# Kernel tuning notes

Measured on AMD Instinct MI355X. Metric: run time of the kernel, lower is better.

## Reference

```python
import jax, jax.numpy as jnp
import numpy as np

N_NODES = 100000
SELF_LOOP_W = 2.0  # improved=True in GCNConv -> A + 2I


def gcn_conv(x, src, dst, ew, W, b):
    """PyG GCNConv(improved=True): D^-1/2 (A + 2I) D^-1/2 X W + b.

    src/dst: edge endpoints, messages flow src -> dst (source_to_target).
    """
    n = x.shape[0]
    # degree after adding self loops with weight 2.0
    deg = jnp.zeros((n,), dtype=x.dtype).at[dst].add(ew) + SELF_LOOP_W
    dinv = jax.lax.rsqrt(deg)
    norm = dinv[src] * ew * dinv[dst]                      # [E]
    h = x @ W                                              # [N, out]
    agg = jax.ops.segment_sum(norm[:, None] * h[src], dst, num_segments=n)
    self_term = (SELF_LOOP_W * dinv * dinv)[:, None] * h   # self-loop edges
    return agg + self_term + b


def setup_inputs() -> dict:
    key = jax.random.key(0)
    ks = jax.random.split(key, 10)
    F_IN, H1, H2, C = 128, 128, 64, 5
    E = 1600000
    x = jax.random.normal(ks[0], (N_NODES, F_IN), dtype=jnp.float32)
    edge_index = jax.random.randint(ks[1], (2, E), 0, N_NODES, dtype=jnp.int64)
    edge_weight = jax.random.uniform(ks[2], (E,), dtype=jnp.float32)

    def glorot(k, shape):
        lim = float(np.sqrt(6.0 / (shape[0] + shape[1])))
        return jax.random.uniform(k, shape, jnp.float32, -lim, lim)

    return {
        "x": x,
        "edge_index": edge_index,
        "edge_weight": edge_weight,
        "W1": glorot(ks[3], (F_IN, H1)), "b1": jnp.zeros((H1,), jnp.float32),
        "W2": glorot(ks[4], (H1, H2)),  "b2": jnp.zeros((H2,), jnp.float32),
        "Wc": glorot(ks[5], (H2, C)),   "bc": jnp.zeros((C,), jnp.float32),
    }


def reference(x, edge_index, edge_weight, W1, b1, W2, b2, Wc, bc):
    src, dst = edge_index[0], edge_index[1]
    # conv1 + relu (dropout is identity in eval mode)
    h = jax.nn.relu(gcn_conv(x, src, dst, edge_weight, W1, b1))
    # conv2 + relu
    h = jax.nn.relu(gcn_conv(h, src, dst, edge_weight, W2, b2))
    # classifier head + log_softmax over classes
    logits = gcn_conv(h, src, dst, edge_weight, Wc, bc)
    return jax.nn.log_softmax(logits, axis=1)
```

## Files before the change

kernel.cpp:

```cpp
#include <hip/hip_runtime.h>
#include <hip/hip_bf16.h>

constexpr int TPB = 256;

static inline int cdiv(long long a, long long b) { return (int)((a + b - 1) / b); }

typedef __attribute__((ext_vector_type(8))) short bf16x8;
typedef __attribute__((ext_vector_type(4))) float f32x4;

__device__ inline unsigned short f2bf(float f) {
    __hip_bfloat16 h = __float2bfloat16(f);
    unsigned short u;
    __builtin_memcpy(&u, &h, 2);
    return u;
}

__device__ inline float bflo(unsigned u) { return __uint_as_float(u << 16); }
__device__ inline float bfhi(unsigned u) { return __uint_as_float(u & 0xffff0000u); }

__device__ inline unsigned relu_pk(unsigned w) {
    unsigned lo = (w & 0x8000u) ? 0u : (w & 0xFFFFu);
    unsigned hi = (w & 0x80000000u) ? 0u : (w & 0xFFFF0000u);
    return lo | hi;
}

constexpr int P1_CH   = 4096;
constexpr int MAXBINS = 512;
constexpr int BINCAP  = 4608;

__device__ __forceinline__ void part_body(const int* __restrict__ src,
                                          const int* __restrict__ dst,
                                          const float* __restrict__ ew,
                                          int* __restrict__ bincnt,
                                          int2* __restrict__ pbuf, int E, int nbins, int bid) {
    __shared__ int h[MAXBINS];
    for (int t = threadIdx.x; t < nbins; t += TPB) h[t] = 0;
    __syncthreads();
    const int lo = bid * P1_CH;
    const int hi = min(lo + P1_CH, E);
    for (int e = lo + threadIdx.x; e < hi; e += TPB)
        atomicAdd(&h[dst[e] >> 8], 1);
    __syncthreads();
    for (int t = threadIdx.x; t < nbins; t += TPB) {
        int c = h[t];
        h[t] = (c > 0) ? atomicAdd(&bincnt[t], c) : 0;
    }
    __syncthreads();
    for (int e = lo + threadIdx.x; e < hi; e += TPB) {
        int d = dst[e];
        int bin = d >> 8;
        int idx = atomicAdd(&h[bin], 1);
        if (idx < BINCAP)
            pbuf[(size_t)bin * BINCAP + idx] =
                make_int2((src[e] & 0x1FFFF) | ((d & 255) << 24), __float_as_int(ew[e]));
    }
}

template<int CAP>
__global__ __launch_bounds__(TPB) void k_bucket(const int2* __restrict__ pbuf,
                                                const int* __restrict__ bincnt,
                                                int2* __restrict__ pairs,
                                                int* __restrict__ cnt,
                                                float* __restrict__ dinv, int n) {
    __shared__ int   lcnt[TPB];
    __shared__ float ldeg[TPB];
    const int tid = threadIdx.x;
    lcnt[tid] = 0; ldeg[tid] = 0.f;
    __syncthreads();
    const int bin = blockIdx.x;
    const int m = min(bincnt[bin], BINCAP);
    const int2* pb = pbuf + (size_t)bin * BINCAP;
    for (int i = tid; i < m; i += TPB) {
        int2 pe = pb[i];
        int dlo = (pe.x >> 24) & 255;
        int s   = pe.x & 0x1FFFF;
        int pos = atomicAdd(&lcnt[dlo], 1);
        if (pos < CAP)
            pairs[(size_t)(bin * 256 + dlo) * CAP + pos] = make_int2(s, pe.y);
        atomicAdd(&ldeg[dlo], __int_as_float(pe.y));
    }
    __syncthreads();
    int node = bin * 256 + tid;
    if (node < n) {
        cnt[node]  = min(lcnt[tid], CAP);
        dinv[node] = rsqrtf(ldeg[tid] + 2.0f);
    }
}

template<int CAP>
__global__ void k_bucket_scatter(const int* __restrict__ src, const int* __restrict__ dst,
                                 const float* __restrict__ ew, int* __restrict__ cnt,
                                 int2* __restrict__ pairs, int E) {
    int e = blockIdx.x * TPB + threadIdx.x;
    if (e >= E) return;
    int d = dst[e];
    int pos = atomicAdd(&cnt[d], 1);
    if (pos < CAP)
        pairs[(size_t)d * CAP + pos] = make_int2(src[e], __float_as_int(ew[e]));
}

template<int CAP>
__global__ void k_deg(const int2* __restrict__ pairs, const int* __restrict__ cnt,
                      float* __restrict__ dinv, int n) {
    int node = blockIdx.x * (TPB / 64) + (threadIdx.x >> 6);
    if (node >= n) return;
    int lane = threadIdx.x & 63;
    int m = min(cnt[node], CAP);
    float v = 0.f;
    if (lane < m) v = __int_as_float(pairs[(size_t)node * CAP + lane].y);
#pragma unroll
    for (int d = 1; d < 64; d <<= 1) v += __shfl_xor(v, d);
    if (lane == 0) dinv[node] = rsqrtf(v + 2.0f);
}

template<int CAP>
__global__ void k_normw(int2* __restrict__ pairs, const int* __restrict__ cnt,
                        const float* __restrict__ dinv, int n) {
    int lane = threadIdx.x & 63;
    int g = lane >> 4, o = lane & 15;
    int wid = blockIdx.x * (TPB / 64) + (threadIdx.x >> 6);
    int node = wid * 4 + g;
    if (node >= n) return;
    int m = min(cnt[node], CAP);
    float dd = dinv[node];
    int2* pr = pairs + (size_t)node * CAP;
    for (int j = o; j < m; j += 16) {
        int2 p = pr[j];
        pr[j].y = __float_as_int(dinv[p.x] * __int_as_float(p.y) * dd);
    }
}

__global__ void k_prepw(const float* __restrict__ W1, const float* __restrict__ W2,
                        __hip_bfloat16* __restrict__ Wt1, __hip_bfloat16* __restrict__ Wt2) {
    int i = blockIdx.x * TPB + threadIdx.x;
    if (i < 128 * 128) {
        int k = i >> 7, c = i & 127;
        Wt1[c * 128 + k] = __float2bfloat16(W1[i]);
    }
    if (i < 128 * 64) {
        int k = i >> 6, c = i & 63;
        Wt2[c * 128 + k] = __float2bfloat16(W2[i]);
    }
}


template<int KIN, int NCOL, bool RELU_IN, bool BF_IN>
__device__ __forceinline__ void gemm_mfma_body(const void* __restrict__ Xv,
                                               const __hip_bfloat16* __restrict__ Wt,
                                               __hip_bfloat16* __restrict__ H, int n, int bid) {
    constexpr int BM  = 128;
    constexpr int SX  = KIN + 8;
    constexpr int KCH = KIN / 32;
    constexpr int MT  = 4;
    constexpr int NT  = NCOL / 32;
    __shared__ short Xs[BM * SX];
    __shared__ short Ws[NCOL * SX];

    const int row0 = bid * BM;
    const int nrow = min(BM, n - row0);

    if constexpr (BF_IN) {
        const uint4* xg = (const uint4*)((const __hip_bfloat16*)Xv + (size_t)row0 * KIN);
        for (int i = threadIdx.x; i < BM * KIN / 8; i += TPB) {
            int r = i / (KIN / 8), c8 = i % (KIN / 8);
            uint4 v = make_uint4(0u, 0u, 0u, 0u);
            if (r < nrow) v = xg[i];
            if (RELU_IN) {
                v.x = relu_pk(v.x); v.y = relu_pk(v.y);
                v.z = relu_pk(v.z); v.w = relu_pk(v.w);
            }
            *(uint4*)&Xs[r * SX + c8 * 8] = v;
        }
    } else {
        const float4* xg = (const float4*)((const float*)Xv + (size_t)row0 * KIN);
        for (int i = threadIdx.x; i < BM * KIN / 4; i += TPB) {
            int r = i / (KIN / 4), c4 = i % (KIN / 4);
            float4 v = make_float4(0.f, 0.f, 0.f, 0.f);
            if (r < nrow) v = xg[i];
            if (RELU_IN) {
                v.x = fmaxf(v.x, 0.f); v.y = fmaxf(v.y, 0.f);
                v.z = fmaxf(v.z, 0.f); v.w = fmaxf(v.w, 0.f);
            }
            ushort4 b;
            b.x = f2bf(v.x); b.y = f2bf(v.y);
            b.z = f2bf(v.z); b.w = f2bf(v.w);
            *(ushort4*)&Xs[r * SX + c4 * 4] = b;
        }
    }
    {
        const uint4* wg = (const uint4*)Wt;
        for (int i = threadIdx.x; i < NCOL * KIN / 8; i += TPB) {
            int c = i / (KIN / 8), k8 = i % (KIN / 8);
            *(uint4*)&Ws[c * SX + k8 * 8] = wg[i];
        }
    }
    __syncthreads();

    const int wave = threadIdx.x >> 6;
    const int lane = threadIdx.x & 63;
    const int wr = wave >> 1;
    const int wc = wave & 1;
    const int fr = lane & 15;
    const int fg = lane >> 4;

    f32x4 acc[MT][NT];
#pragma unroll
    for (int i = 0; i < MT; ++i)
#pragma unroll
        for (int j = 0; j < NT; ++j) acc[i][j] = (f32x4){0.f, 0.f, 0.f, 0.f};

    const short* xa = Xs + (wr * 64 + fr) * SX + fg * 8;
    const short* wb = Ws + (wc * NT * 16 + fr) * SX + fg * 8;

#pragma unroll
    for (int kc = 0; kc < KCH; ++kc) {
        bf16x8 a[MT], b[NT];
#pragma unroll
        for (int i = 0; i < MT; ++i)
            a[i] = *(const bf16x8*)(xa + i * 16 * SX + kc * 32);
#pragma unroll
        for (int j = 0; j < NT; ++j)
            b[j] = *(const bf16x8*)(wb + j * 16 * SX + kc * 32);
#pragma unroll
        for (int i = 0; i < MT; ++i)
#pragma unroll
            for (int j = 0; j < NT; ++j)
                acc[i][j] = __builtin_amdgcn_mfma_f32_16x16x32_bf16(a[i], b[j], acc[i][j], 0, 0, 0);
    }

#pragma unroll
    for (int i = 0; i < MT; ++i) {
#pragma unroll
        for (int j = 0; j < NT; ++j) {
            int col = wc * NT * 16 + j * 16 + fr;
            int rb  = wr * 64 + i * 16 + fg * 4;
#pragma unroll
            for (int q = 0; q < 4; ++q) {
                int r = rb + q;
                if (r < nrow)
                    H[(size_t)(row0 + r) * NCOL + col] = __float2bfloat16(acc[i][j][q]);
            }
        }
    }
}

template<int KIN, int NCOL, bool RELU_IN, bool BF_IN>
__global__ __launch_bounds__(TPB, 2) void k_gemm_mfma(const void* __restrict__ Xv,
                                                      const __hip_bfloat16* __restrict__ Wt,
                                                      __hip_bfloat16* __restrict__ H, int n) {
    gemm_mfma_body<KIN, NCOL, RELU_IN, BF_IN>(Xv, Wt, H, n, blockIdx.x);
}

__global__ __launch_bounds__(TPB, 2) void k_gemm1_part(
        const float* __restrict__ X, const __hip_bfloat16* __restrict__ Wt1,
        __hip_bfloat16* __restrict__ H, int n,
        const int* __restrict__ src, const int* __restrict__ dst,
        const float* __restrict__ ew, int* __restrict__ bincnt,
        int2* __restrict__ pbuf, int E, int nbins, int Gg, int Gp) {
    int b = blockIdx.x;
    int r3 = b % 3;
    if (r3 == 2) {
        int pid = b / 3;
        if (pid < Gp) part_body(src, dst, ew, bincnt, pbuf, E, nbins, pid);
    } else {
        int gid = (b / 3) * 2 + r3;
        if (gid < Gg) gemm_mfma_body<128, 128, false, false>(X, Wt1, H, n, gid);
    }
}

template<int KIN, int KOUT, int OSTR, bool RELU_IN>
__global__ void k_gemv(const float* __restrict__ X, const float* __restrict__ W,
                       float* __restrict__ H, int n) {
    __shared__ float ws_[KIN * KOUT];
    for (int i = threadIdx.x; i < KIN * KOUT; i += TPB) ws_[i] = W[i];
    __syncthreads();
    int r = blockIdx.x * TPB + threadIdx.x;
    if (r >= n) return;
    float acc[KOUT];
#pragma unroll
    for (int c = 0; c < KOUT; ++c) acc[c] = 0.f;
    const float4* xr = (const float4*)(X + (size_t)r * KIN);
#pragma unroll
    for (int k4 = 0; k4 < KIN / 4; ++k4) {
        float4 xv = xr[k4];
        if (RELU_IN) {
            xv.x = fmaxf(xv.x, 0.f); xv.y = fmaxf(xv.y, 0.f);
            xv.z = fmaxf(xv.z, 0.f); xv.w = fmaxf(xv.w, 0.f);
        }
        float xs[4] = {xv.x, xv.y, xv.z, xv.w};
#pragma unroll
        for (int j = 0; j < 4; ++j)
#pragma unroll
            for (int c = 0; c < KOUT; ++c)
                acc[c] = fmaf(xs[j], ws_[(k4 * 4 + j) * KOUT + c], acc[c]);
    }
#pragma unroll
    for (int c = 0; c < KOUT; ++c) H[(size_t)r * OSTR + c] = acc[c];
#pragma unroll
    for (int c = KOUT; c < OSTR; ++c) H[(size_t)r * OSTR + c] = 0.f;
}


template<int K, int CAP, bool OUT_BF16>
__global__ __launch_bounds__(TPB) void k_agg_bf(const __hip_bfloat16* __restrict__ H,
                                                const int2* __restrict__ pairs,
                                                const int* __restrict__ cnt,
                                                const float* __restrict__ dinv,
                                                const float* __restrict__ b,
                                                void* __restrict__ out, int n) {
    constexpr int LPN = K / 8;
    constexpr int GPN = 64 / LPN;
    constexpr int RQ  = K / 8;
    constexpr int NCH = CAP / 8;
    const int lane = threadIdx.x & 63;
    const int g    = lane / LPN;
    const int o    = lane % LPN;
    const int wid  = blockIdx.x * (TPB / 64) + (threadIdx.x >> 6);
    const int node = wid * GPN + g;
    const bool alive = node < n;
    const int nc = alive ? node : 0;

    const uint4* __restrict__ Hq = (const uint4*)H;

    float di   = dinv[nc];
    float coef = 2.f * di * di;
    uint4 hv = Hq[(size_t)nc * RQ + o];
    const float4* bq = (const float4*)b + o * 2;
    float4 bA = bq[0], bB = bq[1];
    float acc[8];
    acc[0] = fmaf(coef, bflo(hv.x), bA.x);
    acc[1] = fmaf(coef, bfhi(hv.x), bA.y);
    acc[2] = fmaf(coef, bflo(hv.y), bA.z);
    acc[3] = fmaf(coef, bfhi(hv.y), bA.w);
    acc[4] = fmaf(coef, bflo(hv.z), bB.x);
    acc[5] = fmaf(coef, bfhi(hv.z), bB.y);
    acc[6] = fmaf(coef, bflo(hv.w), bB.z);
    acc[7] = fmaf(coef, bfhi(hv.w), bB.w);

    const int m = alive ? min(cnt[nc], CAP) : 0;
    const int2* pp = pairs + (size_t)nc * CAP;

    uint4 Ma[4], Mb[4];
#pragma unroll
    for (int q = 0; q < 4; ++q) Ma[q] = *(const uint4*)(pp + q * 2);

    auto chunk = [&](const uint4 (&Mc)[4], uint4 (&Mn)[4], int c) {
        const int base = c * 8;
        int s[8]; float w[8];
#pragma unroll
        for (int q = 0; q < 4; ++q) {
            s[2 * q]     = (int)Mc[q].x;  w[2 * q]     = __uint_as_float(Mc[q].y);
            s[2 * q + 1] = (int)Mc[q].z;  w[2 * q + 1] = __uint_as_float(Mc[q].w);
        }
        uint4 r[8];
#pragma unroll
        for (int u = 0; u < 8; ++u) {
            bool ok = (base + u) < m;
            int ss = ok ? s[u] : 0;
            if (!ok) w[u] = 0.f;
            r[u] = Hq[(size_t)ss * RQ + o];
        }
        if (base + 8 < m) {
#pragma unroll
            for (int q = 0; q < 4; ++q) Mn[q] = *(const uint4*)(pp + base + 8 + q * 2);
        }
#pragma unroll
        for (int u = 0; u < 8; ++u) {
            acc[0] = fmaf(w[u], bflo(r[u].x), acc[0]);
            acc[1] = fmaf(w[u], bfhi(r[u].x), acc[1]);
            acc[2] = fmaf(w[u], bflo(r[u].y), acc[2]);
            acc[3] = fmaf(w[u], bfhi(r[u].y), acc[3]);
            acc[4] = fmaf(w[u], bflo(r[u].z), acc[4]);
            acc[5] = fmaf(w[u], bfhi(r[u].z), acc[5]);
            acc[6] = fmaf(w[u], bflo(r[u].w), acc[6]);
            acc[7] = fmaf(w[u], bfhi(r[u].w), acc[7]);
        }
    };

#pragma unroll
    for (int c = 0; c < NCH; c += 2) {
        if (c * 8 >= m) break;
        chunk(Ma, Mb, c);
        if ((c + 1) * 8 >= m) break;
        chunk(Mb, Ma, c + 1);
    }

    if (alive) {
        if constexpr (OUT_BF16) {
            unsigned p0 = (unsigned)f2bf(acc[0]) | ((unsigned)f2bf(acc[1]) << 16);
            unsigned p1 = (unsigned)f2bf(acc[2]) | ((unsigned)f2bf(acc[3]) << 16);
            unsigned p2 = (unsigned)f2bf(acc[4]) | ((unsigned)f2bf(acc[5]) << 16);
            unsigned p3 = (unsigned)f2bf(acc[6]) | ((unsigned)f2bf(acc[7]) << 16);
            ((uint4*)out)[(size_t)node * RQ + o] = make_uint4(p0, p1, p2, p3);
        } else {
            float4* ap = (float4*)out + (size_t)node * (K / 4) + o * 2;
            ap[0] = make_float4(acc[0], acc[1], acc[2], acc[3]);
            ap[1] = make_float4(acc[4], acc[5], acc[6], acc[7]);
        }
    }
}

template<int CAP>
__global__ void k_agg5_lsm(const float* __restrict__ H, const int2* __restrict__ pairs,
                           const int* __restrict__ cnt, const float* __restrict__ dinv,
                           const float* __restrict__ b, float* __restrict__ out, int n) {
    constexpr int NCH = CAP / 8;
    int i = blockIdx.x * TPB + threadIdx.x;
    const bool alive = i < n;
    const int nc = alive ? i : 0;
    float di = dinv[nc];
    float coef = 2.f * di * di;
    float acc[5];
    {
        const float4 h0 = *(const float4*)(H + (size_t)nc * 8);
        const float  h4 = H[(size_t)nc * 8 + 4];
        acc[0] = fmaf(coef, h0.x, b[0]);
        acc[1] = fmaf(coef, h0.y, b[1]);
        acc[2] = fmaf(coef, h0.z, b[2]);
        acc[3] = fmaf(coef, h0.w, b[3]);
        acc[4] = fmaf(coef, h4,   b[4]);
    }
    const int m = alive ? min(cnt[nc], CAP) : 0;
    const int2* pp = pairs + (size_t)nc * CAP;

    uint4 Ma[4], Mb[4];
#pragma unroll
    for (int q = 0; q < 4; ++q) Ma[q] = *(const uint4*)(pp + q * 2);

    auto chunk = [&](const uint4 (&Mc)[4], uint4 (&Mn)[4], int c) {
        const int base = c * 8;
        int s[8]; float w[8];
#pragma unroll
        for (int q = 0; q < 4; ++q) {
            s[2 * q]     = (int)Mc[q].x;  w[2 * q]     = __uint_as_float(Mc[q].y);
            s[2 * q + 1] = (int)Mc[q].z;  w[2 * q + 1] = __uint_as_float(Mc[q].w);
        }
        float4 q0[8]; float q4[8];
#pragma unroll
        for (int u = 0; u < 8; ++u) {
            bool ok = (base + u) < m;
            int ss = ok ? s[u] : 0;
            if (!ok) w[u] = 0.f;
            const float* h = H + (size_t)ss * 8;
            q0[u] = *(const float4*)h;
            q4[u] = h[4];
        }
        if (base + 8 < m) {
#pragma unroll
            for (int q = 0; q < 4; ++q) Mn[q] = *(const uint4*)(pp + base + 8 + q * 2);
        }
#pragma unroll
        for (int u = 0; u < 8; ++u) {
            acc[0] = fmaf(w[u], q0[u].x, acc[0]);
            acc[1] = fmaf(w[u], q0[u].y, acc[1]);
            acc[2] = fmaf(w[u], q0[u].z, acc[2]);
            acc[3] = fmaf(w[u], q0[u].w, acc[3]);
            acc[4] = fmaf(w[u], q4[u],   acc[4]);
        }
    };

#pragma unroll
    for (int c = 0; c < NCH; c += 2) {
        if (c * 8 >= m) break;
        chunk(Ma, Mb, c);
        if ((c + 1) * 8 >= m) break;
        chunk(Mb, Ma, c + 1);
    }

    if (alive) {
        float mx = acc[0];
#pragma unroll
        for (int c = 1; c < 5; ++c) mx = fmaxf(mx, acc[c]);
        float ssum = 0.f;
#pragma unroll
        for (int c = 0; c < 5; ++c) ssum += expf(acc[c] - mx);
        float lg = mx + logf(ssum);
#pragma unroll
        for (int c = 0; c < 5; ++c) out[(size_t)i * 5 + c] = acc[c] - lg;
    }
}


template<int CAP>
static void run_all(const float* x, const int* srcv, const int* dstv, const float* ew,
                    const float* W1, const float* b1, const float* W2, const float* b2,
                    const float* Wc, const float* bc, float* out,
                    int n, int E, char* p, hipStream_t stream) {
    auto alloc = [&](size_t bytes) {
        char* r = p;
        p += (bytes + 255) & ~(size_t)255;
        return r;
    };
    float*          dinv   = (float*)alloc((size_t)n * 4);
    int*            cnt    = (int*)alloc((size_t)n * 4);
    int2*           pairs  = (int2*)alloc((size_t)n * CAP * 8);
    __hip_bfloat16* Hbf    = (__hip_bfloat16*)alloc((size_t)n * 128 * 2);
    __hip_bfloat16* A1bf   = (__hip_bfloat16*)alloc((size_t)n * 128 * 2);
    float*          bufB   = (float*)alloc((size_t)n * 64 * 4);
    float*          H3     = (float*)alloc((size_t)n * 8 * 4);
    int*            bincnt = (int*)alloc((size_t)MAXBINS * 4);
    int2*           pbuf   = (int2*)alloc((size_t)MAXBINS * BINCAP * 8);
    __hip_bfloat16* Wt1    = (__hip_bfloat16*)alloc(128 * 128 * 2);
    __hip_bfloat16* Wt2    = (__hip_bfloat16*)alloc(128 * 64 * 2);

    const int WPB = TPB / 64;
    const int nbins = cdiv(n, 256);

    k_prepw<<<cdiv(128 * 128, TPB), TPB, 0, stream>>>(W1, W2, Wt1, Wt2);

    if (nbins <= MAXBINS) {
        (void)hipMemsetAsync(bincnt, 0, (size_t)nbins * 4, stream);
        int Gg = cdiv(n, 128);
        int Gp = cdiv(E, P1_CH);
        int Gh = cdiv(Gg, 2);
        int G  = 3 * (Gp > Gh ? Gp : Gh);
        k_gemm1_part<<<G, TPB, 0, stream>>>(x, Wt1, Hbf, n, srcv, dstv, ew,
                                            bincnt, pbuf, E, nbins, Gg, Gp);
        k_bucket<CAP><<<nbins, TPB, 0, stream>>>(pbuf, bincnt, pairs, cnt, dinv, n);
    } else {
        (void)hipMemsetAsync(cnt, 0, (size_t)n * 4, stream);
        k_bucket_scatter<CAP><<<cdiv(E, TPB), TPB, 0, stream>>>(srcv, dstv, ew, cnt, pairs, E);
        k_deg<CAP><<<cdiv(n, WPB), TPB, 0, stream>>>(pairs, cnt, dinv, n);
        k_gemm_mfma<128, 128, false, false><<<cdiv(n, 128), TPB, 0, stream>>>(x, Wt1, Hbf, n);
    }
    k_normw<CAP><<<cdiv(n, WPB * 4), TPB, 0, stream>>>(pairs, cnt, dinv, n);

    k_agg_bf<128, CAP, true><<<cdiv(n, WPB * 4), TPB, 0, stream>>>(Hbf, pairs, cnt, dinv, b1, A1bf, n);

    k_gemm_mfma<128, 64, true, true><<<cdiv(n, 128), TPB, 0, stream>>>(A1bf, Wt2, Hbf, n);
    k_agg_bf<64, CAP, false><<<cdiv(n, WPB * 8), TPB, 0, stream>>>(Hbf, pairs, cnt, dinv, b2, bufB, n);

    k_gemv<64, 5, 8, true><<<cdiv(n, TPB), TPB, 0, stream>>>(bufB, Wc, H3, n);
    k_agg5_lsm<CAP><<<cdiv(n, TPB), TPB, 0, stream>>>(H3, pairs, cnt, dinv, bc, out, n);
}

extern "C" void kernel_launch(void* const* d_in, const int* in_sizes, int n_in,
                              void* d_out, int out_size, void* d_ws, size_t ws_size,
                              hipStream_t stream) {
    const float* x  = (const float*)d_in[0];
    const int*   ei = (const int*)d_in[1];
    const float* ew = (const float*)d_in[2];
    const float* W1 = (const float*)d_in[3];
    const float* b1 = (const float*)d_in[4];
    const float* W2 = (const float*)d_in[5];
    const float* b2 = (const float*)d_in[6];
    const float* Wc = (const float*)d_in[7];
    const float* bc = (const float*)d_in[8];

    const int E   = in_sizes[2];
    const int H1  = in_sizes[4];
    const int FIN = in_sizes[3] / H1;
    const int n   = in_sizes[0] / FIN;

    const int* srcv = ei;
    const int* dstv = ei + E;

    size_t fixed = ((size_t)n * 4 + 256) * 2 + ((size_t)n * 128 * 2 + 256) * 2 +
                   (size_t)n * 64 * 4 + 256 + (size_t)n * 8 * 4 + 256 +
                   (size_t)MAXBINS * 4 + 256 + (size_t)MAXBINS * BINCAP * 8 + 256 +
                   128 * 128 * 2 + 256 + 128 * 64 * 2 + 256 + 1024;
    if (ws_size == 0 || ws_size >= fixed + (size_t)n * 64 * 8)
        run_all<64>(x, srcv, dstv, ew, W1, b1, W2, b2, Wc, bc, (float*)d_out, n, E,
                    (char*)d_ws, stream);
    else
        run_all<48>(x, srcv, dstv, ew, W1, b1, W2, b2, Wc, bc, (float*)d_out, n, E,
                    (char*)d_ws, stream);
}
```

Before: 216.7 us.

## Load GEMM weights directly from global with register prefetch, cut LDS, raise occupancy

Drops the shared-memory staging of the weight matrix in the MFMA GEMM. B fragments are now read directly from global (L2-cached) memory, with a one-step register double buffer. The fused gemm+partition kernel shares a single LDS buffer between its two roles, and launch bounds go from 2 to 4 blocks per SM to raise occupancy. The trade-off is more global and L2 traffic per wave and more register pressure under the tighter launch bound.

```diff
diff --git a/kernel.cpp b/kernel.cpp
--- a/kernel.cpp
+++ b/kernel.cpp
@@ -32,8 +32,8 @@
                                           const int* __restrict__ dst,
                                           const float* __restrict__ ew,
                                           int* __restrict__ bincnt,
-                                          int2* __restrict__ pbuf, int E, int nbins, int bid) {
-    __shared__ int h[MAXBINS];
+                                          int2* __restrict__ pbuf, int E, int nbins,
+                                          int* h, int bid) {
     for (int t = threadIdx.x; t < nbins; t += TPB) h[t] = 0;
     __syncthreads();
     const int lo = bid * P1_CH;
@@ -147,14 +147,13 @@
 template<int KIN, int NCOL, bool RELU_IN, bool BF_IN>
 __device__ __forceinline__ void gemm_mfma_body(const void* __restrict__ Xv,
                                                const __hip_bfloat16* __restrict__ Wt,
-                                               __hip_bfloat16* __restrict__ H, int n, int bid) {
+                                               __hip_bfloat16* __restrict__ H, int n,
+                                               int bid, short* Xs) {
     constexpr int BM  = 128;
     constexpr int SX  = KIN + 8;
     constexpr int KCH = KIN / 32;
     constexpr int MT  = 4;
     constexpr int NT  = NCOL / 32;
-    __shared__ short Xs[BM * SX];
-    __shared__ short Ws[NCOL * SX];
 
     const int row0 = bid * BM;
     const int nrow = min(BM, n - row0);
@@ -187,13 +186,6 @@
             *(ushort4*)&Xs[r * SX + c4 * 4] = b;
         }
     }
-    {
-        const uint4* wg = (const uint4*)Wt;
-        for (int i = threadIdx.x; i < NCOL * KIN / 8; i += TPB) {
-            int c = i / (KIN / 8), k8 = i % (KIN / 8);
-            *(uint4*)&Ws[c * SX + k8 * 8] = wg[i];
-        }
-    }
     __syncthreads();
 
     const int wave = threadIdx.x >> 6;
@@ -210,22 +202,33 @@
         for (int j = 0; j < NT; ++j) acc[i][j] = (f32x4){0.f, 0.f, 0.f, 0.f};
 
     const short* xa = Xs + (wr * 64 + fr) * SX + fg * 8;
-    const short* wb = Ws + (wc * NT * 16 + fr) * SX + fg * 8;
+    const __hip_bfloat16* wg = Wt + (size_t)(wc * NT * 16 + fr) * KIN + fg * 8;
+
+    bf16x8 bcur[NT], bnxt[NT];
+#pragma unroll
+    for (int j = 0; j < NT; ++j)
+        bcur[j] = *(const bf16x8*)(wg + (size_t)j * 16 * KIN);
 
 #pragma unroll
     for (int kc = 0; kc < KCH; ++kc) {
-        bf16x8 a[MT], b[NT];
+        bf16x8 a[MT];
 #pragma unroll
         for (int i = 0; i < MT; ++i)
             a[i] = *(const bf16x8*)(xa + i * 16 * SX + kc * 32);
-#pragma unroll
-        for (int j = 0; j < NT; ++j)
-            b[j] = *(const bf16x8*)(wb + j * 16 * SX + kc * 32);
+        if (kc + 1 < KCH) {
+#pragma unroll
+            for (int j = 0; j < NT; ++j)
+                bnxt[j] = *(const bf16x8*)(wg + (size_t)j * 16 * KIN + (kc + 1) * 32);
+        }
 #pragma unroll
         for (int i = 0; i < MT; ++i)
 #pragma unroll
             for (int j = 0; j < NT; ++j)
-                acc[i][j] = __builtin_amdgcn_mfma_f32_16x16x32_bf16(a[i], b[j], acc[i][j], 0, 0, 0);
+                acc[i][j] = __builtin_amdgcn_mfma_f32_16x16x32_bf16(a[i], bcur[j], acc[i][j], 0, 0, 0);
+        if (kc + 1 < KCH) {
+#pragma unroll
+            for (int j = 0; j < NT; ++j) bcur[j] = bnxt[j];
+        }
     }
 
 #pragma unroll
@@ -245,26 +248,28 @@
 }
 
 template<int KIN, int NCOL, bool RELU_IN, bool BF_IN>
-__global__ __launch_bounds__(TPB, 2) void k_gemm_mfma(const void* __restrict__ Xv,
+__global__ __launch_bounds__(TPB, 4) void k_gemm_mfma(const void* __restrict__ Xv,
                                                       const __hip_bfloat16* __restrict__ Wt,
                                                       __hip_bfloat16* __restrict__ H, int n) {
-    gemm_mfma_body<KIN, NCOL, RELU_IN, BF_IN>(Xv, Wt, H, n, blockIdx.x);
-}
-
-__global__ __launch_bounds__(TPB, 2) void k_gemm1_part(
+    __shared__ __align__(16) short Xs[128 * (KIN + 8)];
+    gemm_mfma_body<KIN, NCOL, RELU_IN, BF_IN>(Xv, Wt, H, n, blockIdx.x, Xs);
+}
+
+__global__ __launch_bounds__(TPB, 4) void k_gemm1_part(
         const float* __restrict__ X, const __hip_bfloat16* __restrict__ Wt1,
         __hip_bfloat16* __restrict__ H, int n,
         const int* __restrict__ src, const int* __restrict__ dst,
         const float* __restrict__ ew, int* __restrict__ bincnt,
         int2* __restrict__ pbuf, int E, int nbins, int Gg, int Gp) {
+    __shared__ __align__(16) short smem[128 * 136];
     int b = blockIdx.x;
     int r3 = b % 3;
     if (r3 == 2) {
         int pid = b / 3;
-        if (pid < Gp) part_body(src, dst, ew, bincnt, pbuf, E, nbins, pid);
+        if (pid < Gp) part_body(src, dst, ew, bincnt, pbuf, E, nbins, (int*)smem, pid);
     } else {
         int gid = (b / 3) * 2 + r3;
-        if (gid < Gg) gemm_mfma_body<128, 128, false, false>(X, Wt1, H, n, gid);
+        if (gid < Gg) gemm_mfma_body<128, 128, false, false>(X, Wt1, H, n, gid, smem);
     }
 }
 
```

After: 216.2 us. About the same (-0.2%).
